# Performance work log

Hardware: AMD Instinct MI355X
Metric: run time of the kernel (lower is better)

Reference implementation:

```python
import jax, jax.numpy as jnp
import numpy as np

N_NODES = 50000
N_EDGES = 300000
MUL0 = 16          # multiplicity of 0e in irreps_in/out
MUL1 = 8           # multiplicity of 1o in irreps_in/out
SCAL_OUT = MUL0 + MUL1   # 24 = true scalars + gate scalars (tp scalar output)
DIM_IN = MUL0 + 3 * MUL1  # 40
W_NUMEL = MUL0 * SCAL_OUT + MUL1 * SCAL_OUT + MUL0 * MUL1 + MUL1 * MUL1  # 768
SQRT3 = float(np.sqrt(3.0))
ALPHA = float(1.0 / np.sqrt(MUL0 + MUL1))  # e3nn 'element' path norm: fan_in = 16*1 + 8*1 = 24
BN_EPS = 1e-5


def setup_inputs() -> dict:
    key = jax.random.key(0)
    ks = jax.random.split(key, 16)
    f32 = jnp.float32
    return {
        "node_features": jax.random.normal(ks[0], (N_NODES, DIM_IN), f32),
        "edge_sh": jax.random.normal(ks[1], (N_EDGES, 4), f32),
        "edge_basis": jax.random.uniform(ks[2], (N_EDGES, 8), dtype=f32),
        "edge_index": jax.random.randint(ks[3], (2, N_EDGES), 0, N_NODES),
        # radial MLP params (8 -> 64 -> 64 -> 768)
        "W1": jax.random.normal(ks[4], (8, 64), f32) / np.sqrt(8.0),
        "b1": jnp.zeros((64,), f32),
        "W2": jax.random.normal(ks[5], (64, 64), f32) / np.sqrt(64.0),
        "b2": jnp.zeros((64,), f32),
        "W3": jax.random.normal(ks[6], (64, W_NUMEL), f32) / np.sqrt(64.0),
        "b3": jnp.zeros((W_NUMEL,), f32),
        # o3.Linear (self-interaction) weights, block diagonal per irrep
        "si_w0": jax.random.normal(ks[7], (MUL0, MUL0), f32),
        "si_w1": jax.random.normal(ks[8], (MUL1, MUL1), f32),
        # e3nn BatchNorm affine params
        "bn_ws": jnp.ones((MUL0,), f32),
        "bn_bs": jnp.zeros((MUL0,), f32),
        "bn_wv": jnp.ones((MUL1,), f32),
    }


def _radial_mlp(basis, W1, b1, W2, b2, W3, b3):
    h = jax.nn.silu(basis @ W1 + b1)
    h = jax.nn.silu(h @ W2 + b2)
    return h @ W3 + b3  # (E, W_NUMEL)


def reference(node_features, edge_sh, edge_basis, edge_index,
              W1, b1, W2, b2, W3, b3, si_w0, si_w1, bn_ws, bn_bs, bn_wv):
    src, dst = edge_index[0], edge_index[1]
    E = edge_sh.shape[0]

    tp_w = _radial_mlp(edge_basis, W1, b1, W2, b2, W3, b3)  # (E, 768)
    o0 = MUL0 * SCAL_OUT                     # 384
    o1 = o0 + MUL1 * SCAL_OUT                # 576
    o2 = o1 + MUL0 * MUL1                    # 704
    w_ss = tp_w[:, :o0].reshape(E, MUL0, SCAL_OUT)   # 0e x 0e -> 0e
    w_vv = tp_w[:, o0:o1].reshape(E, MUL1, SCAL_OUT)  # 1o x 1o -> 0e
    w_sv = tp_w[:, o1:o2].reshape(E, MUL0, MUL1)      # 0e x 1o -> 1o
    w_vs = tp_w[:, o2:].reshape(E, MUL1, MUL1)        # 1o x 0e -> 1o

    # gather source node features
    feats = node_features[src]                          # (E, 40)
    sx = feats[:, :MUL0]                                # (E, 16)
    vx = feats[:, MUL0:].reshape(E, MUL1, 3)            # (E, 8, 3)
    sh0 = edge_sh[:, 0:1]                               # (E, 1)
    sh1 = edge_sh[:, 1:4]                               # (E, 3)

    # scalar output channels (true scalars + gate scalars), component-normalized CG
    dot_vv = jnp.einsum('eui,ei->eu', vx, sh1) / SQRT3  # 1o.1o -> 0e CG
    out_s = (jnp.einsum('eu,euw->ew', sx * sh0, w_ss)
             + jnp.einsum('eu,euw->ew', dot_vv, w_vv)) * ALPHA   # (E, 24)

    # vector (1o) output channels
    out_v = (jnp.einsum('eu,ei,euw->ewi', sx, sh1, w_sv)
             + jnp.einsum('eui,euw->ewi', vx * sh0[:, :, None], w_vs)) * ALPHA  # (E, 8, 3)

    messages = jnp.concatenate([out_s, out_v.reshape(E, 3 * MUL1)], axis=-1)  # (E, 48)

    # scatter-add to destination nodes
    agg = jax.ops.segment_sum(messages, dst, num_segments=node_features.shape[0])  # (N, 48)

    # Gate: SiLU on true scalars, sigmoid gate scalars modulate 1o irreps
    s = jax.nn.silu(agg[:, :MUL0])                       # (N, 16)
    g = jax.nn.sigmoid(agg[:, MUL0:SCAL_OUT])            # (N, 8)
    v = agg[:, SCAL_OUT:].reshape(-1, MUL1, 3) * g[:, :, None]  # (N, 8, 3)

    # self-interaction: o3.Linear, block-diagonal per irrep, 1/sqrt(fan_in) scaling
    s = s @ (si_w0 / np.sqrt(MUL0))                      # (N, 16)
    v = jnp.einsum('nui,uw->nwi', v, si_w1 / np.sqrt(MUL1))  # (N, 8, 3)

    # e3nn BatchNorm (training stats, component normalization, affine)
    s = s - jnp.mean(s, axis=0)
    s_norm = jnp.mean(s * s, axis=0)                     # (16,)
    s = s * jax.lax.rsqrt(s_norm + BN_EPS) * bn_ws + bn_bs
    v_norm = jnp.mean(jnp.mean(v * v, axis=-1), axis=0)  # (8,) per-mul mean sq component
    v = v * (jax.lax.rsqrt(v_norm + BN_EPS) * bn_wv)[None, :, None]

    out = jnp.concatenate([s, v.reshape(-1, 3 * MUL1)], axis=-1)  # (N, 40)
    return out + node_features  # residual (irreps_in == irreps_out)
```

## Files before the change

### kernel.cpp

```cpp
#include <hip/hip_runtime.h>
#include <hip/hip_bf16.h>


#define N_NODES_C 50000
#define N_EDGES_C 300000
#define ALPHA_C 0.20412414523193154f
#define INV_SQRT3_C 0.5773502691896258f
#define BN_EPS_C 1e-5f

typedef unsigned int u32;
typedef unsigned long long u64;
typedef unsigned short u16;
typedef __attribute__((ext_vector_type(8))) short bf16x8;
typedef __attribute__((ext_vector_type(4))) float f32x4;

#define OFF_STATS 0u
#define OFF_FLAG  48u
#define OFF_W3T   64u
#define OFF_W1T   49216u
#define OFF_B1    49728u
#define OFF_W2T   49792u
#define OFF_B2    53888u
#define OFF_B3    53952u
#define OFF_SI0   54720u
#define OFF_SI1   54976u
#define OFF_AGG   55040u
#define REQ_WS_BYTES ((size_t)(55040u + 2400000u) * 4u)
#define OFF_SPART   2455040u
#define OFF_START   2505040u
#define OFF_CURSOR  2555044u
#define OFF_POS     2605044u
#define OFF_MSG     2905044u
#define REQ2_WS_BYTES ((size_t)(2905044u + 14400000u) * 4u)

#define GATHER_BLOCKS ((N_NODES_C + 63) / 64)

__device__ __forceinline__ float bflo(u32 u){ union{u32 i; float f;} c; c.i = u<<16; return c.f; }
__device__ __forceinline__ float bfhi(u32 u){ union{u32 i; float f;} c; c.i = u & 0xffff0000u; return c.f; }
__device__ __forceinline__ float b2f(__hip_bfloat16 b){ return (float)b; }
__device__ __forceinline__ u16 f2bf(float f){
    union{float f; u32 i;} c; c.f = f;
    u32 r = c.i + 0x7fffu + ((c.i>>16)&1u);
    return (u16)(r>>16);
}
__device__ __forceinline__ float sigmoidf_(float x){ return 1.0f/(1.0f+__expf(-x)); }
__device__ __forceinline__ float siluf_(float x){ return x*sigmoidf_(x); }
__device__ __forceinline__ float rdv(const void* p, int idx, bool fm){
    return fm ? ((const float*)p)[idx] : b2f(((const __hip_bfloat16*)p)[idx]);
}
__device__ __forceinline__ float sel4(float a, float b, float c, float d, int q){
    float lo = (q&1) ? b : a;
    float hi = (q&1) ? d : c;
    return (q&2) ? hi : lo;
}
__device__ __forceinline__ float sel8(float a0,float a1,float a2,float a3,
                                      float a4,float a5,float a6,float a7,int q){
    float x0=(q&1)?a1:a0, x1=(q&1)?a3:a2, x2=(q&1)?a5:a4, x3=(q&1)?a7:a6;
    float y0=(q&2)?x1:x0, y1=(q&2)?x3:x2;
    return (q&4)?y1:y0;
}
__device__ __forceinline__ void wave_fence(){
    asm volatile("s_waitcnt lgkmcnt(0)" ::: "memory");
}

__global__ __launch_bounds__(256) void fill_kernel(u32* __restrict__ p, int n, u32 v){
    int i = blockIdx.x*256 + threadIdx.x;
    if (i < n) p[i] = v;
}

__global__ __launch_bounds__(256) void prep_kernel(
    const void* __restrict__ nf,
    const void* __restrict__ W1, const void* __restrict__ b1,
    const void* __restrict__ W2, const void* __restrict__ b2,
    const void* __restrict__ W3, const void* __restrict__ b3,
    const void* __restrict__ si0, const void* __restrict__ si1,
    float* __restrict__ ws)
{
    __shared__ u32 fmsh;
    {
        const int t = threadIdx.x;
        if (t < 64){
            u32 w = ((const u32*)nf)[t];
            int bad = 0;
            u32 lo = w & 0xffffu, hi = w >> 16;
            u32 elo = (lo >> 7) & 0xffu, ehi = (hi >> 7) & 0xffu;
            if (!(lo == 0u || (elo >= 90u && elo <= 140u))) bad++;
            if (!(hi == 0u || (ehi >= 90u && ehi <= 140u))) bad++;
            for (int off=32; off; off>>=1) bad += __shfl_down(bad, off);
            if (t == 0) fmsh = (bad >= 8) ? 1u : 0u;
        }
        __syncthreads();
    }
    const bool fm = fmsh != 0u;
    if (blockIdx.x == 0 && threadIdx.x == 0) ((u32*)(ws + OFF_FLAG))[0] = fm ? 1u : 0u;

    int i = blockIdx.x*256 + threadIdx.x;
    if (i < 49152){
        int j = i & 7, lane = (i>>3)&63, kh = (i>>9)&1, nt = i>>10;
        int n = lane & 15, qd = lane >> 4;
        int k = kh*32 + qd*8 + j;
        int col = nt*16 + n;
        float v = rdv(W3, k*768 + col, fm);
        u16 hv = f2bf(v);
        float hf = bflo((u32)hv);
        u16 lv = f2bf(v - hf);
        u16* BH = (u16*)(ws + OFF_W3T);
        BH[i] = hv;
        BH[49152 + i] = lv;
        return;
    }
    i -= 49152;
    if (i < 512){ int j=i>>3, t=i&7; ws[OFF_W1T+i] = rdv(W1, t*64+j, fm); return; }
    i -= 512;
    if (i < 64){ ws[OFF_B1+i] = rdv(b1, i, fm); return; }
    i -= 64;
    if (i < 4096){ int j=i>>6, k=i&63; ws[OFF_W2T+i] = rdv(W2, k*64+j, fm); return; }
    i -= 4096;
    if (i < 64){ ws[OFF_B2+i] = rdv(b2, i, fm); return; }
    i -= 64;
    if (i < 768){ ws[OFF_B3+i] = rdv(b3, i, fm); return; }
    i -= 768;
    if (i < 256){ int w=i>>4, u=i&15; ws[OFF_SI0+i] = rdv(si0, u*16+w, fm)*0.25f; return; }
    i -= 256;
    if (i < 64){ int w=i>>3, u=i&7; ws[OFF_SI1+i] = rdv(si1, u*8+w, fm)*0.35355339059327373f; return; }
}

__global__ __launch_bounds__(256) void rank_kernel(const int* __restrict__ dst,
                                                   int* __restrict__ cursor,
                                                   int* __restrict__ rank){
    int i = blockIdx.x*256 + threadIdx.x;
    if (i < N_EDGES_C){
        rank[i] = atomicAdd(&cursor[dst[i]], 1);
    }
}

__global__ __launch_bounds__(1024) void scan_kernel(const int* __restrict__ deg,
                                                    int* __restrict__ start){
    __shared__ int buf[2][1024];
    const int t = threadIdx.x;
    const int c0 = t*49;
    int local = 0;
    #pragma unroll 1
    for (int i=0;i<49;i++){ int idx=c0+i; if (idx<N_NODES_C) local += deg[idx]; }
    buf[0][t] = local;
    __syncthreads();
    int src=0;
    for (int off=1; off<1024; off<<=1){
        int v = buf[src][t];
        if (t>=off) v += buf[src][t-off];
        buf[src^1][t]=v;
        src^=1;
        __syncthreads();
    }
    int off = (t==0)?0:buf[src][t-1];
    #pragma unroll 1
    for (int i=0;i<49;i++){
        int idx=c0+i;
        if (idx<N_NODES_C){ start[idx]=off; off+=deg[idx]; }
    }
    if (t==0) start[N_NODES_C]=buf[src][1023];
}

__global__ __launch_bounds__(256) void pos_kernel(const int* __restrict__ dst,
                                                  const int* __restrict__ start,
                                                  int* __restrict__ rankpos){
    int i = blockIdx.x*256 + threadIdx.x;
    if (i < N_EDGES_C){
        rankpos[i] = start[dst[i]] + rankpos[i];
    }
}

template<bool SORTED>
__global__ __launch_bounds__(128, 2) void edge_kernel_t(
    const void* __restrict__ nfv,
    const void* __restrict__ eshv,
    const void* __restrict__ ebv,
    const int* __restrict__ eidx,
    const float* __restrict__ ws,
    const int* __restrict__ pos,
    float* __restrict__ outbuf)
{
    __shared__ __align__(16) char uni[2][12544];
    const int wv   = threadIdx.x >> 6;
    const int lane = threadIdx.x & 63;
    u16   (*h2hi)[72] = (u16 (*)[72])uni[wv];
    float (*tpb)[49]  = (float (*)[49])uni[wv];

    const bool fm = ((const u32*)(ws + OFF_FLAG))[0] != 0u;
    const int m    = lane & 15;
    const int quad = lane >> 4;
    const int e    = blockIdx.x*128 + threadIdx.x;
    const bool act = e < N_EDGES_C;
    const int slot = (SORTED && act) ? pos[e] : 0;

    float sh0=0.f, sh1x=0.f, sh1y=0.f, sh1z=0.f;
    float f[40];
    float bas[8];
    #pragma unroll
    for (int i=0;i<40;i++) f[i]=0.f;
    #pragma unroll
    for (int i=0;i<8;i++) bas[i]=0.f;
    if (act){
        const int src = eidx[e];
        if (!fm){
            const u32* p = (const u32*)((const __hip_bfloat16*)eshv + (size_t)e*4);
            u32 a = p[0], b = p[1];
            sh0 = bflo(a); sh1x = bfhi(a); sh1y = bflo(b); sh1z = bfhi(b);
            const uint4* qq = (const uint4*)((const __hip_bfloat16*)nfv + (size_t)src*40);
            #pragma unroll
            for (int i=0;i<5;i++){
                uint4 r = qq[i];
                f[i*8+0]=bflo(r.x); f[i*8+1]=bfhi(r.x);
                f[i*8+2]=bflo(r.y); f[i*8+3]=bfhi(r.y);
                f[i*8+4]=bflo(r.z); f[i*8+5]=bfhi(r.z);
                f[i*8+6]=bflo(r.w); f[i*8+7]=bfhi(r.w);
            }
            uint4 r = *(const uint4*)((const __hip_bfloat16*)ebv + (size_t)e*8);
            bas[0]=bflo(r.x); bas[1]=bfhi(r.x); bas[2]=bflo(r.y); bas[3]=bfhi(r.y);
            bas[4]=bflo(r.z); bas[5]=bfhi(r.z); bas[6]=bflo(r.w); bas[7]=bfhi(r.w);
        } else {
            float4 r = *(const float4*)((const float*)eshv + (size_t)e*4);
            sh0 = r.x; sh1x = r.y; sh1y = r.z; sh1z = r.w;
            const float4* qq = (const float4*)((const float*)nfv + (size_t)src*40);
            #pragma unroll
            for (int i=0;i<10;i++){
                float4 t = qq[i];
                f[i*4+0]=t.x; f[i*4+1]=t.y; f[i*4+2]=t.z; f[i*4+3]=t.w;
            }
            const float4* qb = (const float4*)((const float*)ebv + (size_t)e*8);
            float4 t0 = qb[0], t1 = qb[1];
            bas[0]=t0.x; bas[1]=t0.y; bas[2]=t0.z; bas[3]=t0.w;
            bas[4]=t1.x; bas[5]=t1.y; bas[6]=t1.z; bas[7]=t1.w;
        }
    }

    const float* W1T = ws + OFF_W1T;
    const float* b1f = ws + OFF_B1;
    float h1[64];
    #pragma unroll
    for (int j=0;j<64;j++){
        const float* w = W1T + j*8;
        float t0 = b1f[j] + bas[0]*w[0] + bas[4]*w[4];
        float t1 = bas[1]*w[1] + bas[5]*w[5];
        float t2 = bas[2]*w[2] + bas[6]*w[6];
        float t3 = bas[3]*w[3] + bas[7]*w[7];
        h1[j] = siluf_((t0+t1)+(t2+t3));
    }

    const float* W2T = ws + OFF_W2T;
    const float* bb2 = ws + OFF_B2;
    #pragma unroll 1
    for (int j=0;j<64;j+=2){
        const float* w0 = W2T + j*64;
        const float* w1 = w0 + 64;
        float a0=bb2[j],   a1=0.f, a2=0.f, a3=0.f;
        float c0=bb2[j+1], c1=0.f, c2=0.f, c3=0.f;
        #pragma unroll
        for (int k=0;k<64;k+=4){
            a0 += h1[k]*w0[k];     a1 += h1[k+1]*w0[k+1];
            a2 += h1[k+2]*w0[k+2]; a3 += h1[k+3]*w0[k+3];
            c0 += h1[k]*w1[k];     c1 += h1[k+1]*w1[k+1];
            c2 += h1[k+2]*w1[k+2]; c3 += h1[k+3]*w1[k+3];
        }
        u32 pk = (u32)f2bf(siluf_((a0+a1)+(a2+a3)))
               | ((u32)f2bf(siluf_((c0+c1)+(c2+c3)))<<16);
        *(u32*)&h2hi[lane][j] = pk;
    }
    wave_fence();

    bf16x8 Afr[4][2];
    #pragma unroll
    for (int g=0;g<4;g++){
        Afr[g][0] = *(const bf16x8*)&h2hi[g*16+m][quad*8];
        Afr[g][1] = *(const bf16x8*)&h2hi[g*16+m][32 + quad*8];
    }
    wave_fence();

    float vxsh0[24], dvv[8];
    #pragma unroll
    for (int j=0;j<24;j++) vxsh0[j] = f[16+j]*sh0;
    #pragma unroll
    for (int u=0;u<8;u++)
        dvv[u] = (f[16+u*3]*sh1x + f[17+u*3]*sh1y + f[18+u*3]*sh1z)*INV_SQRT3_C;

    float outs[24], tsv[8], av0[8], av1[8], av2[8];
    #pragma unroll
    for (int t=0;t<24;t++) outs[t]=0.f;
    #pragma unroll
    for (int t=0;t<8;t++){ tsv[t]=0.f; av0[t]=0.f; av1[t]=0.f; av2[t]=0.f; }

    const short* BH = (const short*)(ws + OFF_W3T);
    const float* b3f = ws + OFF_B3;

    auto loadB = [&](bf16x8* dst2, int cc2){
        #pragma unroll
        for (int ntl=0; ntl<3; ntl++){
            const int nt = cc2*3 + ntl;
            dst2[ntl*2+0] = *(const bf16x8*)(BH + ((nt*2+0)*64 + lane)*8);
            dst2[ntl*2+1] = *(const bf16x8*)(BH + ((nt*2+1)*64 + lane)*8);
        }
    };

    bf16x8 Bc[6];
    loadB(Bc, 0);

    #pragma unroll 1
    for (int cc=0; cc<16; cc++){
        #pragma unroll
        for (int ntl=0; ntl<3; ntl++){
            #pragma unroll
            for (int g=0; g<4; g++){
                f32x4 acc = {0.f,0.f,0.f,0.f};
                acc = __builtin_amdgcn_mfma_f32_16x16x32_bf16(Afr[g][0], Bc[ntl*2+0], acc, 0,0,0);
                acc = __builtin_amdgcn_mfma_f32_16x16x32_bf16(Afr[g][1], Bc[ntl*2+1], acc, 0,0,0);
                #pragma unroll
                for (int r=0;r<4;r++) tpb[g*16+quad*4+r][ntl*16+m] = acc[r];
            }
        }
        if (cc < 15) loadB(Bc, cc+1);
        wave_fence();

        float cA=0.f, cB=0.f;
        if (cc < 8){
            cA = sel8(f[0],f[2],f[4],f[6],f[8],f[10],f[12],f[14], cc)*sh0;
            cB = sel8(f[1],f[3],f[5],f[7],f[9],f[11],f[13],f[15], cc)*sh0;
        } else if (cc < 12){
            cA = sel4(dvv[0],dvv[2],dvv[4],dvv[6], cc-8);
            cB = sel4(dvv[1],dvv[3],dvv[5],dvv[7], cc-8);
        }
        const float* b3c = b3f + cc*48;
        float v[16];

        #pragma unroll
        for (int c=0;c<16;c++) v[c] = tpb[lane][c] + b3c[c];
        if (cc < 12){
            #pragma unroll
            for (int c=0;c<16;c++) outs[c] += cA*v[c];
        } else if (cc == 12){
            #pragma unroll
            for (int c=0;c<16;c++) tsv[c&7] += f[c>>3]*v[c];
        } else if (cc == 13){
            #pragma unroll
            for (int c=0;c<16;c++) tsv[c&7] += f[6+(c>>3)]*v[c];
        } else if (cc == 14){
            #pragma unroll
            for (int c=0;c<16;c++) tsv[c&7] += f[12+(c>>3)]*v[c];
        } else {
            #pragma unroll
            for (int c=0;c<16;c++){
                const int u=2+(c>>3), w=c&7;
                av0[w] += vxsh0[u*3+0]*v[c];
                av1[w] += vxsh0[u*3+1]*v[c];
                av2[w] += vxsh0[u*3+2]*v[c];
            }
        }

        #pragma unroll
        for (int c=0;c<16;c++) v[c] = tpb[lane][16+c] + b3c[16+c];
        if (cc < 12){
            #pragma unroll
            for (int c=0;c<8;c++)  outs[16+c] += cA*v[c];
            #pragma unroll
            for (int c=8;c<16;c++) outs[c-8]  += cB*v[c];
        } else if (cc == 12){
            #pragma unroll
            for (int c=0;c<16;c++) tsv[c&7] += f[2+(c>>3)]*v[c];
        } else if (cc == 13){
            #pragma unroll
            for (int c=0;c<16;c++) tsv[c&7] += f[8+(c>>3)]*v[c];
        } else if (cc == 14){
            #pragma unroll
            for (int c=0;c<16;c++) tsv[c&7] += f[14+(c>>3)]*v[c];
        } else {
            #pragma unroll
            for (int c=0;c<16;c++){
                const int u=4+(c>>3), w=c&7;
                av0[w] += vxsh0[u*3+0]*v[c];
                av1[w] += vxsh0[u*3+1]*v[c];
                av2[w] += vxsh0[u*3+2]*v[c];
            }
        }

        #pragma unroll
        for (int c=0;c<16;c++) v[c] = tpb[lane][32+c] + b3c[32+c];
        if (cc < 12){
            #pragma unroll
            for (int c=0;c<16;c++) outs[8+c] += cB*v[c];
        } else if (cc == 12){
            #pragma unroll
            for (int c=0;c<16;c++) tsv[c&7] += f[4+(c>>3)]*v[c];
        } else if (cc == 13){
            #pragma unroll
            for (int c=0;c<16;c++) tsv[c&7] += f[10+(c>>3)]*v[c];
        } else if (cc == 14){
            #pragma unroll
            for (int c=0;c<16;c++){
                const int u=(c>>3), w=c&7;
                av0[w] += vxsh0[u*3+0]*v[c];
                av1[w] += vxsh0[u*3+1]*v[c];
                av2[w] += vxsh0[u*3+2]*v[c];
            }
        } else {
            #pragma unroll
            for (int c=0;c<16;c++){
                const int u=6+(c>>3), w=c&7;
                av0[w] += vxsh0[u*3+0]*v[c];
                av1[w] += vxsh0[u*3+1]*v[c];
                av2[w] += vxsh0[u*3+2]*v[c];
            }
        }
        wave_fence();
    }

    if (act){
        if (SORTED){
            float v48[48];
            #pragma unroll
            for (int w=0;w<24;w++) v48[w] = outs[w]*ALPHA_C;
            #pragma unroll
            for (int w=0;w<8;w++){
                v48[24+w*3+0] = (tsv[w]*sh1x + av0[w])*ALPHA_C;
                v48[24+w*3+1] = (tsv[w]*sh1y + av1[w])*ALPHA_C;
                v48[24+w*3+2] = (tsv[w]*sh1z + av2[w])*ALPHA_C;
            }
            float4* mp = (float4*)(outbuf + (size_t)slot*48);
            #pragma unroll
            for (int q=0;q<12;q++) mp[q] = make_float4(v48[q*4],v48[q*4+1],v48[q*4+2],v48[q*4+3]);
        } else {
            const int dst = eidx[N_EDGES_C + e];
            float* dp = outbuf + (size_t)dst*48;
            #pragma unroll
            for (int w=0;w<24;w++) atomicAdd(dp+w, outs[w]*ALPHA_C);
            #pragma unroll
            for (int w=0;w<8;w++){
                atomicAdd(dp+24+w*3+0, (tsv[w]*sh1x + av0[w])*ALPHA_C);
                atomicAdd(dp+24+w*3+1, (tsv[w]*sh1y + av1[w])*ALPHA_C);
                atomicAdd(dp+24+w*3+2, (tsv[w]*sh1z + av2[w])*ALPHA_C);
            }
        }
    }
}

__global__ __launch_bounds__(512) void gather_node_kernel(
    const float* __restrict__ ws,
    const float* __restrict__ msg,
    const int* __restrict__ start,
    float* __restrict__ svb,
    float* __restrict__ spart)
{
    __shared__ __align__(16) float aggL[64][52];
    const float* si0T = ws + OFF_SI0;
    const float* si1T = ws + OFF_SI1;
    const int tid = threadIdx.x;
    const int nb = blockIdx.x*64;
    {
        const int sub  = tid & 3;
        const int rsp  = (tid >> 2) & 1;
        const int slot = tid >> 3;
        const int n = nb + slot;
        float a[12], b[12];
        #pragma unroll
        for (int i=0;i<12;i++){ a[i]=0.f; b[i]=0.f; }
        if (n < N_NODES_C){
            const int s = start[n], en = start[n+1];
            #pragma unroll 1
            for (int r = s + rsp; r < en; r += 4){
                const float4* mp = (const float4*)(msg + (size_t)r*48) + sub*3;
                float4 t0=mp[0], t1=mp[1], t2=mp[2];
                const int r2 = r + 2;
                if (r2 < en){
                    const float4* mq = (const float4*)(msg + (size_t)r2*48) + sub*3;
                    float4 u0=mq[0], u1=mq[1], u2=mq[2];
                    b[0]+=u0.x; b[1]+=u0.y; b[2]+=u0.z; b[3]+=u0.w;
                    b[4]+=u1.x; b[5]+=u1.y; b[6]+=u1.z; b[7]+=u1.w;
                    b[8]+=u2.x; b[9]+=u2.y; b[10]+=u2.z; b[11]+=u2.w;
                }
                a[0]+=t0.x; a[1]+=t0.y; a[2]+=t0.z; a[3]+=t0.w;
                a[4]+=t1.x; a[5]+=t1.y; a[6]+=t1.z; a[7]+=t1.w;
                a[8]+=t2.x; a[9]+=t2.y; a[10]+=t2.z; a[11]+=t2.w;
            }
        }
        #pragma unroll
        for (int i=0;i<12;i++) a[i] += b[i];
        #pragma unroll
        for (int i=0;i<12;i++) a[i] += __shfl_xor(a[i], 4);
        if (rsp == 0){
            float4* dp = (float4*)&aggL[slot][sub*12];
            dp[0]=make_float4(a[0],a[1],a[2],a[3]);
            dp[1]=make_float4(a[4],a[5],a[6],a[7]);
            dp[2]=make_float4(a[8],a[9],a[10],a[11]);
        }
    }
    __syncthreads();
    if (tid >= 64) return;
    const int n = nb + tid;
    const bool act = n < N_NODES_C;

    float a[48];
    {
        const float4* p = (const float4*)&aggL[tid][0];
        #pragma unroll
        for (int q=0;q<12;q++){ float4 r=p[q]; a[q*4]=r.x; a[q*4+1]=r.y; a[q*4+2]=r.z; a[q*4+3]=r.w; }
    }
    float spre[16];
    #pragma unroll
    for (int u=0;u<16;u++) spre[u]=siluf_(a[u]);
    float v[24];
    #pragma unroll
    for (int u=0;u<8;u++){
        float g = sigmoidf_(a[16+u]);
        v[u*3+0]=a[24+u*3+0]*g; v[u*3+1]=a[24+u*3+1]*g; v[u*3+2]=a[24+u*3+2]*g;
    }
    float so[16];
    #pragma unroll
    for (int w=0;w<16;w++){
        const float* c = si0T + w*16;
        float t0=0.f,t1=0.f,t2=0.f,t3=0.f;
        #pragma unroll
        for (int u=0;u<16;u+=4){ t0+=spre[u]*c[u]; t1+=spre[u+1]*c[u+1]; t2+=spre[u+2]*c[u+2]; t3+=spre[u+3]*c[u+3]; }
        so[w]=(t0+t1)+(t2+t3);
    }
    float vo[24];
    #pragma unroll
    for (int w=0;w<8;w++){
        const float* c = si1T + w*8;
        float a0=0.f,a1=0.f,a2=0.f;
        #pragma unroll
        for (int u=0;u<8;u++){ a0+=v[u*3]*c[u]; a1+=v[u*3+1]*c[u]; a2+=v[u*3+2]*c[u]; }
        vo[w*3]=a0; vo[w*3+1]=a1; vo[w*3+2]=a2;
    }
    if (act){
        float4* op = (float4*)(svb + (size_t)n*48);
        op[0]=make_float4(so[0],so[1],so[2],so[3]);
        op[1]=make_float4(so[4],so[5],so[6],so[7]);
        op[2]=make_float4(so[8],so[9],so[10],so[11]);
        op[3]=make_float4(so[12],so[13],so[14],so[15]);
        #pragma unroll
        for (int q=0;q<6;q++) op[4+q]=make_float4(vo[q*4],vo[q*4+1],vo[q*4+2],vo[q*4+3]);
    }
    float r[40];
    #pragma unroll
    for (int w=0;w<16;w++){ r[w]=so[w]; r[16+w]=so[w]*so[w]; }
    #pragma unroll
    for (int w=0;w<8;w++) r[32+w]=(vo[w*3]*vo[w*3]+vo[w*3+1]*vo[w*3+1]+vo[w*3+2]*vo[w*3+2])*(1.0f/3.0f);
    #pragma unroll
    for (int j=0;j<40;j++){
        float x = r[j];
        for (int off=32; off; off>>=1) x += __shfl_down(x, off);
        r[j]=x;
    }
    if (tid==0){
        float* sp = spart + (size_t)blockIdx.x*40;
        #pragma unroll
        for (int q=0;q<10;q++)
            *(float4*)(sp + q*4) = make_float4(r[q*4],r[q*4+1],r[q*4+2],r[q*4+3]);
    }
}

__global__ __launch_bounds__(1024) void reduce_stats_kernel(
    const float* __restrict__ spart, int nblk, float* __restrict__ stats)
{
    const int tid = threadIdx.x;
    if (tid >= 640) return;
    const int c = tid >> 4;
    const int l = tid & 15;
    float s = 0.f;
    #pragma unroll 1
    for (int k = l; k < nblk; k += 16) s += spart[(size_t)k*40 + c];
    #pragma unroll
    for (int off=8; off; off>>=1) s += __shfl_xor(s, off);
    if (l == 0) stats[c] = s;
}

__global__ __launch_bounds__(256) void node_kernel_atomic(
    const float* __restrict__ ws,
    float* __restrict__ svb,
    float* __restrict__ stats)
{
    const float* si0T = ws + OFF_SI0;
    const float* si1T = ws + OFF_SI1;
    const int n = blockIdx.x*256 + threadIdx.x;
    const bool act = n < N_NODES_C;

    float a[48];
    #pragma unroll
    for (int j=0;j<48;j++) a[j]=0.f;
    if (act){
        const float4* p = (const float4*)(svb + (size_t)n*48);
        #pragma unroll
        for (int q=0;q<12;q++){ float4 r=p[q]; a[q*4]=r.x; a[q*4+1]=r.y; a[q*4+2]=r.z; a[q*4+3]=r.w; }
    }
    float spre[16];
    #pragma unroll
    for (int u=0;u<16;u++) spre[u]=siluf_(a[u]);
    float v[24];
    #pragma unroll
    for (int u=0;u<8;u++){
        float g = sigmoidf_(a[16+u]);
        v[u*3+0]=a[24+u*3+0]*g; v[u*3+1]=a[24+u*3+1]*g; v[u*3+2]=a[24+u*3+2]*g;
    }
    float so[16];
    #pragma unroll
    for (int w=0;w<16;w++){
        const float* c = si0T + w*16;
        float t0=0.f,t1=0.f,t2=0.f,t3=0.f;
        #pragma unroll
        for (int u=0;u<16;u+=4){ t0+=spre[u]*c[u]; t1+=spre[u+1]*c[u+1]; t2+=spre[u+2]*c[u+2]; t3+=spre[u+3]*c[u+3]; }
        so[w]=(t0+t1)+(t2+t3);
    }
    float vo[24];
    #pragma unroll
    for (int w=0;w<8;w++){
        const float* c = si1T + w*8;
        float a0=0.f,a1=0.f,a2=0.f;
        #pragma unroll
        for (int u=0;u<8;u++){ a0+=v[u*3]*c[u]; a1+=v[u*3+1]*c[u]; a2+=v[u*3+2]*c[u]; }
        vo[w*3]=a0; vo[w*3+1]=a1; vo[w*3+2]=a2;
    }
    if (act){
        float4* op = (float4*)(svb + (size_t)n*48);
        op[0]=make_float4(so[0],so[1],so[2],so[3]);
        op[1]=make_float4(so[4],so[5],so[6],so[7]);
        op[2]=make_float4(so[8],so[9],so[10],so[11]);
        op[3]=make_float4(so[12],so[13],so[14],so[15]);
        #pragma unroll
        for (int q=0;q<6;q++) op[4+q]=make_float4(vo[q*4],vo[q*4+1],vo[q*4+2],vo[q*4+3]);
    }
    float r[40];
    #pragma unroll
    for (int w=0;w<16;w++){ r[w]=so[w]; r[16+w]=so[w]*so[w]; }
    #pragma unroll
    for (int w=0;w<8;w++) r[32+w]=(vo[w*3]*vo[w*3]+vo[w*3+1]*vo[w*3+1]+vo[w*3+2]*vo[w*3+2])*(1.0f/3.0f);
    #pragma unroll
    for (int j=0;j<40;j++){
        float x = r[j];
        for (int off=32; off; off>>=1) x += __shfl_down(x, off);
        r[j]=x;
    }
    if ((threadIdx.x & 63)==0){
        #pragma unroll
        for (int j=0;j<40;j++) atomicAdd(stats+j, r[j]);
    }
}

__global__ __launch_bounds__(256) void final_kernel(
    const float* __restrict__ ws, const float* __restrict__ svb,
    const void* __restrict__ nfv,
    const void* __restrict__ bnws, const void* __restrict__ bnbs,
    const void* __restrict__ bnwv,
    void* __restrict__ outv)
{
    const float* stats = ws + OFF_STATS;
    const bool fm = ((const u32*)(ws + OFF_FLAG))[0] != 0u;
    const int n = blockIdx.x*256 + threadIdx.x;
    if (n >= N_NODES_C) return;
    const float invN = 1.0f/(float)N_NODES_C;
    const float* s = svb + (size_t)n*48;
    float nfr[40];
    if (!fm){
        const uint4* q = (const uint4*)((const __hip_bfloat16*)nfv + (size_t)n*40);
        #pragma unroll
        for (int i=0;i<5;i++){
            uint4 r = q[i];
            nfr[i*8+0]=bflo(r.x); nfr[i*8+1]=bfhi(r.x);
            nfr[i*8+2]=bflo(r.y); nfr[i*8+3]=bfhi(r.y);
            nfr[i*8+4]=bflo(r.z); nfr[i*8+5]=bfhi(r.z);
            nfr[i*8+6]=bflo(r.w); nfr[i*8+7]=bfhi(r.w);
        }
    } else {
        const float4* q = (const float4*)((const float*)nfv + (size_t)n*40);
        #pragma unroll
        for (int i=0;i<10;i++){
            float4 t = q[i];
            nfr[i*4+0]=t.x; nfr[i*4+1]=t.y; nfr[i*4+2]=t.z; nfr[i*4+3]=t.w;
        }
    }
    float vals[40];
    #pragma unroll
    for (int w=0;w<16;w++){
        float mean = stats[w]*invN;
        float var  = fmaxf(stats[16+w]*invN - mean*mean, 0.0f);
        float is   = rsqrtf(var + BN_EPS_C) * rdv(bnws, w, fm);
        vals[w] = (s[w]-mean)*is + rdv(bnbs, w, fm) + nfr[w];
    }
    #pragma unroll
    for (int w=0;w<8;w++){
        float iv = rsqrtf(fmaxf(stats[32+w]*invN, 0.0f) + BN_EPS_C) * rdv(bnwv, w, fm);
        vals[16+w*3+0] = s[16+w*3+0]*iv + nfr[16+w*3+0];
        vals[16+w*3+1] = s[16+w*3+1]*iv + nfr[16+w*3+1];
        vals[16+w*3+2] = s[16+w*3+2]*iv + nfr[16+w*3+2];
    }
    if (!fm){
        u32 packed[20];
        #pragma unroll
        for (int q=0;q<20;q++) packed[q] = (u32)f2bf(vals[2*q]) | ((u32)f2bf(vals[2*q+1])<<16);
        uint4* op = (uint4*)((u16*)outv + (size_t)n*40);
        #pragma unroll
        for (int q=0;q<5;q++) op[q] = make_uint4(packed[q*4],packed[q*4+1],packed[q*4+2],packed[q*4+3]);
    } else {
        float4* op = (float4*)((float*)outv + (size_t)n*40);
        #pragma unroll
        for (int q=0;q<10;q++) op[q] = make_float4(vals[q*4],vals[q*4+1],vals[q*4+2],vals[q*4+3]);
    }
}

extern "C" void kernel_launch(void* const* d_in, const int* in_sizes, int n_in,
                              void* d_out, int out_size, void* d_ws, size_t ws_size,
                              hipStream_t stream)
{
    const void* nf     = d_in[0];
    const void* esh    = d_in[1];
    const void* ebasis = d_in[2];
    const int*  eidx   = (const int*)d_in[3];
    const void* W1 = d_in[4];
    const void* b1 = d_in[5];
    const void* W2 = d_in[6];
    const void* b2 = d_in[7];
    const void* W3 = d_in[8];
    const void* b3 = d_in[9];
    const void* si0 = d_in[10];
    const void* si1 = d_in[11];
    const void* bnws = d_in[12];
    const void* bnbs = d_in[13];
    const void* bnwv = d_in[14];

    float* ws    = (float*)d_ws;
    float* stats = ws + OFF_STATS;
    float* agg   = ws + OFF_AGG;

    if (ws_size < REQ_WS_BYTES){
        int nw = out_size/2;
        fill_kernel<<<(nw+255)/256, 256, 0, stream>>>((u32*)d_out, nw, 0x447A447Au);
        return;
    }

    const int* dst = eidx + N_EDGES_C;
    const int EB = (N_EDGES_C+255)/256;
    const int EB128 = (N_EDGES_C+127)/128;

    hipMemsetAsync(stats, 0, 48*sizeof(float), stream);
    prep_kernel<<<215, 256, 0, stream>>>(nf, W1,b1,W2,b2,W3,b3,si0,si1, ws);

    if (ws_size >= REQ2_WS_BYTES){
        int*   startp = (int*)(ws + OFF_START);
        int*   cursor = (int*)(ws + OFF_CURSOR);
        int*   posb   = (int*)(ws + OFF_POS);
        float* spart  = ws + OFF_SPART;
        float* msg    = ws + OFF_MSG;

        hipMemsetAsync(cursor, 0, N_NODES_C*sizeof(int), stream);
        rank_kernel<<<EB, 256, 0, stream>>>(dst, cursor, posb);
        scan_kernel<<<1, 1024, 0, stream>>>(cursor, startp);
        pos_kernel<<<EB, 256, 0, stream>>>(dst, startp, posb);
        edge_kernel_t<true><<<EB128, 128, 0, stream>>>(nf, esh, ebasis, eidx, ws, posb, msg);
        gather_node_kernel<<<GATHER_BLOCKS, 512, 0, stream>>>(ws, msg, startp, agg, spart);
        reduce_stats_kernel<<<1, 1024, 0, stream>>>(spart, GATHER_BLOCKS, stats);
    } else {
        hipMemsetAsync(agg, 0, (size_t)2400000*sizeof(float), stream);
        edge_kernel_t<false><<<EB128, 128, 0, stream>>>(nf, esh, ebasis, eidx, ws, nullptr, agg);
        node_kernel_atomic<<<(N_NODES_C+255)/256, 256, 0, stream>>>(ws, agg, stats);
    }
    final_kernel<<<(N_NODES_C+255)/256, 256, 0, stream>>>(ws, agg, nf, bnws, bnbs, bnwv, d_out);
}
```

Baseline: 500.8 us.

## Permute W3 columns so each chunk yields complete outputs, store per chunk

The W3 and b3 columns are permuted in the prep kernel so that each 48-column MFMA chunk holds every weight needed for two output channels. Each chunk can then reduce to final outputs and write or atomically add them at once, instead of keeping 48 running accumulators across all chunks. The vxsh0 values move to LDS, and the node-feature gather is deferred until after the MLP layers, all to lower register pressure. The cost is extra LDS space, more scattered small stores per chunk, and more LDS reads of vxl.

```diff
diff --git a/kernel.cpp b/kernel.cpp
--- a/kernel.cpp
+++ b/kernel.cpp
@@ -48,16 +48,16 @@
 __device__ __forceinline__ float rdv(const void* p, int idx, bool fm){
     return fm ? ((const float*)p)[idx] : b2f(((const __hip_bfloat16*)p)[idx]);
 }
-__device__ __forceinline__ float sel4(float a, float b, float c, float d, int q){
-    float lo = (q&1) ? b : a;
-    float hi = (q&1) ? d : c;
-    return (q&2) ? hi : lo;
-}
-__device__ __forceinline__ float sel8(float a0,float a1,float a2,float a3,
-                                      float a4,float a5,float a6,float a7,int q){
-    float x0=(q&1)?a1:a0, x1=(q&1)?a3:a2, x2=(q&1)?a5:a4, x3=(q&1)?a7:a6;
-    float y0=(q&2)?x1:x0, y1=(q&2)?x3:x2;
-    return (q&4)?y1:y0;
+__device__ __forceinline__ int w3col(int cc, int c){
+    int kk = (c >= 24) ? (c - 24) : c;
+    int hb = (c >= 24) ? 1 : 0;
+    if (cc < 12){
+        int w = 2*cc + hb;
+        return (kk < 16) ? (kk*24 + w) : (384 + (kk-16)*24 + w);
+    } else {
+        int w = 2*(cc-12) + hb;
+        return (kk < 16) ? (576 + kk*8 + w) : (704 + (kk-16)*8 + w);
+    }
 }
 __device__ __forceinline__ void wave_fence(){
     asm volatile("s_waitcnt lgkmcnt(0)" ::: "memory");
@@ -99,7 +99,8 @@
         int j = i & 7, lane = (i>>3)&63, kh = (i>>9)&1, nt = i>>10;
         int n = lane & 15, qd = lane >> 4;
         int k = kh*32 + qd*8 + j;
-        int col = nt*16 + n;
+        int cc = nt/3, c = (nt%3)*16 + n;
+        int col = w3col(cc, c);
         float v = rdv(W3, k*768 + col, fm);
         u16 hv = f2bf(v);
         float hf = bflo((u32)hv);
@@ -118,7 +119,11 @@
     i -= 4096;
     if (i < 64){ ws[OFF_B2+i] = rdv(b2, i, fm); return; }
     i -= 64;
-    if (i < 768){ ws[OFF_B3+i] = rdv(b3, i, fm); return; }
+    if (i < 768){
+        int cc = i/48, c = i%48;
+        ws[OFF_B3+i] = rdv(b3, w3col(cc, c), fm);
+        return;
+    }
     i -= 768;
     if (i < 256){ int w=i>>4, u=i&15; ws[OFF_SI0+i] = rdv(si0, u*16+w, fm)*0.25f; return; }
     i -= 256;
@@ -180,11 +185,12 @@
     const int* __restrict__ pos,
     float* __restrict__ outbuf)
 {
-    __shared__ __align__(16) char uni[2][12544];
+    __shared__ __align__(16) char uni[2][18688];
     const int wv   = threadIdx.x >> 6;
     const int lane = threadIdx.x & 63;
     u16   (*h2hi)[72] = (u16 (*)[72])uni[wv];
     float (*tpb)[49]  = (float (*)[49])uni[wv];
+    float (*vxl)[64]  = (float (*)[64])(uni[wv] + 12544);
 
     const bool fm = ((const u32*)(ws + OFF_FLAG))[0] != 0u;
     const int m    = lane & 15;
@@ -192,20 +198,70 @@
     const int e    = blockIdx.x*128 + threadIdx.x;
     const bool act = e < N_EDGES_C;
     const int slot = (SORTED && act) ? pos[e] : 0;
+    const int src  = act ? eidx[e] : 0;
+    const int dstn = (!SORTED && act) ? eidx[N_EDGES_C + e] : 0;
 
     float sh0=0.f, sh1x=0.f, sh1y=0.f, sh1z=0.f;
-    float f[40];
     float bas[8];
-    #pragma unroll
-    for (int i=0;i<40;i++) f[i]=0.f;
     #pragma unroll
     for (int i=0;i<8;i++) bas[i]=0.f;
     if (act){
-        const int src = eidx[e];
         if (!fm){
             const u32* p = (const u32*)((const __hip_bfloat16*)eshv + (size_t)e*4);
             u32 a = p[0], b = p[1];
             sh0 = bflo(a); sh1x = bfhi(a); sh1y = bflo(b); sh1z = bfhi(b);
+            uint4 r = *(const uint4*)((const __hip_bfloat16*)ebv + (size_t)e*8);
+            bas[0]=bflo(r.x); bas[1]=bfhi(r.x); bas[2]=bflo(r.y); bas[3]=bfhi(r.y);
+            bas[4]=bflo(r.z); bas[5]=bfhi(r.z); bas[6]=bflo(r.w); bas[7]=bfhi(r.w);
+        } else {
+            float4 r = *(const float4*)((const float*)eshv + (size_t)e*4);
+            sh0 = r.x; sh1x = r.y; sh1y = r.z; sh1z = r.w;
+            const float4* qb = (const float4*)((const float*)ebv + (size_t)e*8);
+            float4 t0 = qb[0], t1 = qb[1];
+            bas[0]=t0.x; bas[1]=t0.y; bas[2]=t0.z; bas[3]=t0.w;
+            bas[4]=t1.x; bas[5]=t1.y; bas[6]=t1.z; bas[7]=t1.w;
+        }
+    }
+
+    const float* W1T = ws + OFF_W1T;
+    const float* b1f = ws + OFF_B1;
+    float h1[64];
+    #pragma unroll
+    for (int j=0;j<64;j++){
+        const float* w = W1T + j*8;
+        float t0 = b1f[j] + bas[0]*w[0] + bas[4]*w[4];
+        float t1 = bas[1]*w[1] + bas[5]*w[5];
+        float t2 = bas[2]*w[2] + bas[6]*w[6];
+        float t3 = bas[3]*w[3] + bas[7]*w[7];
+        h1[j] = siluf_((t0+t1)+(t2+t3));
+    }
+
+    const float* W2T = ws + OFF_W2T;
+    const float* bb2 = ws + OFF_B2;
+    #pragma unroll 1
+    for (int j=0;j<64;j+=2){
+        const float* w0 = W2T + j*64;
+        const float* w1 = w0 + 64;
+        float a0=bb2[j],   a1=0.f, a2=0.f, a3=0.f;
+        float c0=bb2[j+1], c1=0.f, c2=0.f, c3=0.f;
+        #pragma unroll
+        for (int k=0;k<64;k+=4){
+            a0 += h1[k]*w0[k];     a1 += h1[k+1]*w0[k+1];
+            a2 += h1[k+2]*w0[k+2]; a3 += h1[k+3]*w0[k+3];
+            c0 += h1[k]*w1[k];     c1 += h1[k+1]*w1[k+1];
+            c2 += h1[k+2]*w1[k+2]; c3 += h1[k+3]*w1[k+3];
+        }
+        u32 pk = (u32)f2bf(siluf_((a0+a1)+(a2+a3)))
+               | ((u32)f2bf(siluf_((c0+c1)+(c2+c3)))<<16);
+        *(u32*)&h2hi[lane][j] = pk;
+    }
+    wave_fence();
+
+    float f[40];
+    #pragma unroll
+    for (int i=0;i<40;i++) f[i]=0.f;
+    if (act){
+        if (!fm){
             const uint4* qq = (const uint4*)((const __hip_bfloat16*)nfv + (size_t)src*40);
             #pragma unroll
             for (int i=0;i<5;i++){
@@ -215,58 +271,15 @@
                 f[i*8+4]=bflo(r.z); f[i*8+5]=bfhi(r.z);
                 f[i*8+6]=bflo(r.w); f[i*8+7]=bfhi(r.w);
             }
-            uint4 r = *(const uint4*)((const __hip_bfloat16*)ebv + (size_t)e*8);
-            bas[0]=bflo(r.x); bas[1]=bfhi(r.x); bas[2]=bflo(r.y); bas[3]=bfhi(r.y);
-            bas[4]=bflo(r.z); bas[5]=bfhi(r.z); bas[6]=bflo(r.w); bas[7]=bfhi(r.w);
         } else {
-            float4 r = *(const float4*)((const float*)eshv + (size_t)e*4);
-            sh0 = r.x; sh1x = r.y; sh1y = r.z; sh1z = r.w;
             const float4* qq = (const float4*)((const float*)nfv + (size_t)src*40);
             #pragma unroll
             for (int i=0;i<10;i++){
                 float4 t = qq[i];
                 f[i*4+0]=t.x; f[i*4+1]=t.y; f[i*4+2]=t.z; f[i*4+3]=t.w;
             }
-            const float4* qb = (const float4*)((const float*)ebv + (size_t)e*8);
-            float4 t0 = qb[0], t1 = qb[1];
-            bas[0]=t0.x; bas[1]=t0.y; bas[2]=t0.z; bas[3]=t0.w;
-            bas[4]=t1.x; bas[5]=t1.y; bas[6]=t1.z; bas[7]=t1.w;
-        }
-    }
-
-    const float* W1T = ws + OFF_W1T;
-    const float* b1f = ws + OFF_B1;
-    float h1[64];
-    #pragma unroll
-    for (int j=0;j<64;j++){
-        const float* w = W1T + j*8;
-        float t0 = b1f[j] + bas[0]*w[0] + bas[4]*w[4];
-        float t1 = bas[1]*w[1] + bas[5]*w[5];
-        float t2 = bas[2]*w[2] + bas[6]*w[6];
-        float t3 = bas[3]*w[3] + bas[7]*w[7];
-        h1[j] = siluf_((t0+t1)+(t2+t3));
-    }
-
-    const float* W2T = ws + OFF_W2T;
-    const float* bb2 = ws + OFF_B2;
-    #pragma unroll 1
-    for (int j=0;j<64;j+=2){
-        const float* w0 = W2T + j*64;
-        const float* w1 = w0 + 64;
-        float a0=bb2[j],   a1=0.f, a2=0.f, a3=0.f;
-        float c0=bb2[j+1], c1=0.f, c2=0.f, c3=0.f;
-        #pragma unroll
-        for (int k=0;k<64;k+=4){
-            a0 += h1[k]*w0[k];     a1 += h1[k+1]*w0[k+1];
-            a2 += h1[k+2]*w0[k+2]; a3 += h1[k+3]*w0[k+3];
-            c0 += h1[k]*w1[k];     c1 += h1[k+1]*w1[k+1];
-            c2 += h1[k+2]*w1[k+2]; c3 += h1[k+3]*w1[k+3];
-        }
-        u32 pk = (u32)f2bf(siluf_((a0+a1)+(a2+a3)))
-               | ((u32)f2bf(siluf_((c0+c1)+(c2+c3)))<<16);
-        *(u32*)&h2hi[lane][j] = pk;
-    }
-    wave_fence();
+        }
+    }
 
     bf16x8 Afr[4][2];
     #pragma unroll
@@ -276,18 +289,12 @@
     }
     wave_fence();
 
-    float vxsh0[24], dvv[8];
-    #pragma unroll
-    for (int j=0;j<24;j++) vxsh0[j] = f[16+j]*sh0;
+    float dvv[8];
     #pragma unroll
     for (int u=0;u<8;u++)
         dvv[u] = (f[16+u*3]*sh1x + f[17+u*3]*sh1y + f[18+u*3]*sh1z)*INV_SQRT3_C;
-
-    float outs[24], tsv[8], av0[8], av1[8], av2[8];
-    #pragma unroll
-    for (int t=0;t<24;t++) outs[t]=0.f;
-    #pragma unroll
-    for (int t=0;t<8;t++){ tsv[t]=0.f; av0[t]=0.f; av1[t]=0.f; av2[t]=0.f; }
+    #pragma unroll
+    for (int j=0;j<24;j++) vxl[j][lane] = f[16+j]*sh0;
 
     const short* BH = (const short*)(ws + OFF_W3T);
     const float* b3f = ws + OFF_B3;
@@ -303,6 +310,9 @@
 
     bf16x8 Bc[6];
     loadB(Bc, 0);
+
+    float* const mp = SORTED ? (outbuf + (size_t)slot*48)
+                             : (outbuf + (size_t)dstn*48);
 
     #pragma unroll 1
     for (int cc=0; cc<16; cc++){
@@ -320,124 +330,67 @@
         if (cc < 15) loadB(Bc, cc+1);
         wave_fence();
 
-        float cA=0.f, cB=0.f;
-        if (cc < 8){
-            cA = sel8(f[0],f[2],f[4],f[6],f[8],f[10],f[12],f[14], cc)*sh0;
-            cB = sel8(f[1],f[3],f[5],f[7],f[9],f[11],f[13],f[15], cc)*sh0;
-        } else if (cc < 12){
-            cA = sel4(dvv[0],dvv[2],dvv[4],dvv[6], cc-8);
-            cB = sel4(dvv[1],dvv[3],dvv[5],dvv[7], cc-8);
-        }
         const float* b3c = b3f + cc*48;
-        float v[16];
-
-        #pragma unroll
-        for (int c=0;c<16;c++) v[c] = tpb[lane][c] + b3c[c];
         if (cc < 12){
+            float sa0=0.f, sa1=0.f, da0=0.f, da1=0.f;
             #pragma unroll
-            for (int c=0;c<16;c++) outs[c] += cA*v[c];
-        } else if (cc == 12){
+            for (int k=0;k<16;k++){
+                sa0 += f[k]*(tpb[lane][k]    + b3c[k]);
+                sa1 += f[k]*(tpb[lane][24+k] + b3c[24+k]);
+            }
             #pragma unroll
-            for (int c=0;c<16;c++) tsv[c&7] += f[c>>3]*v[c];
-        } else if (cc == 13){
+            for (int k=0;k<8;k++){
+                da0 += dvv[k]*(tpb[lane][16+k] + b3c[16+k]);
+                da1 += dvv[k]*(tpb[lane][40+k] + b3c[40+k]);
+            }
+            float o0 = (sh0*sa0 + da0)*ALPHA_C;
+            float o1 = (sh0*sa1 + da1)*ALPHA_C;
+            if (act){
+                if (SORTED){
+                    *(float2*)(mp + 2*cc) = make_float2(o0, o1);
+                } else {
+                    atomicAdd(mp + 2*cc,     o0);
+                    atomicAdd(mp + 2*cc + 1, o1);
+                }
+            }
+        } else {
+            const int w0 = 2*(cc-12);
+            float t0=0.f, t1=0.f;
+            float a00=0.f,a01=0.f,a02=0.f, a10=0.f,a11=0.f,a12=0.f;
             #pragma unroll
-            for (int c=0;c<16;c++) tsv[c&7] += f[6+(c>>3)]*v[c];
-        } else if (cc == 14){
+            for (int k=0;k<16;k++){
+                t0 += f[k]*(tpb[lane][k]    + b3c[k]);
+                t1 += f[k]*(tpb[lane][24+k] + b3c[24+k]);
+            }
             #pragma unroll
-            for (int c=0;c<16;c++) tsv[c&7] += f[12+(c>>3)]*v[c];
-        } else {
-            #pragma unroll
-            for (int c=0;c<16;c++){
-                const int u=2+(c>>3), w=c&7;
-                av0[w] += vxsh0[u*3+0]*v[c];
-                av1[w] += vxsh0[u*3+1]*v[c];
-                av2[w] += vxsh0[u*3+2]*v[c];
-            }
-        }
-
-        #pragma unroll
-        for (int c=0;c<16;c++) v[c] = tpb[lane][16+c] + b3c[16+c];
-        if (cc < 12){
-            #pragma unroll
-            for (int c=0;c<8;c++)  outs[16+c] += cA*v[c];
-            #pragma unroll
-            for (int c=8;c<16;c++) outs[c-8]  += cB*v[c];
-        } else if (cc == 12){
-            #pragma unroll
-            for (int c=0;c<16;c++) tsv[c&7] += f[2+(c>>3)]*v[c];
-        } else if (cc == 13){
-            #pragma unroll
-            for (int c=0;c<16;c++) tsv[c&7] += f[8+(c>>3)]*v[c];
-        } else if (cc == 14){
-            #pragma unroll
-            for (int c=0;c<16;c++) tsv[c&7] += f[14+(c>>3)]*v[c];
-        } else {
-            #pragma unroll
-            for (int c=0;c<16;c++){
-                const int u=4+(c>>3), w=c&7;
-                av0[w] += vxsh0[u*3+0]*v[c];
-                av1[w] += vxsh0[u*3+1]*v[c];
-                av2[w] += vxsh0[u*3+2]*v[c];
-            }
-        }
-
-        #pragma unroll
-        for (int c=0;c<16;c++) v[c] = tpb[lane][32+c] + b3c[32+c];
-        if (cc < 12){
-            #pragma unroll
-            for (int c=0;c<16;c++) outs[8+c] += cB*v[c];
-        } else if (cc == 12){
-            #pragma unroll
-            for (int c=0;c<16;c++) tsv[c&7] += f[4+(c>>3)]*v[c];
-        } else if (cc == 13){
-            #pragma unroll
-            for (int c=0;c<16;c++) tsv[c&7] += f[10+(c>>3)]*v[c];
-        } else if (cc == 14){
-            #pragma unroll
-            for (int c=0;c<16;c++){
-                const int u=(c>>3), w=c&7;
-                av0[w] += vxsh0[u*3+0]*v[c];
-                av1[w] += vxsh0[u*3+1]*v[c];
-                av2[w] += vxsh0[u*3+2]*v[c];
-            }
-        } else {
-            #pragma unroll
-            for (int c=0;c<16;c++){
-                const int u=6+(c>>3), w=c&7;
-                av0[w] += vxsh0[u*3+0]*v[c];
-                av1[w] += vxsh0[u*3+1]*v[c];
-                av2[w] += vxsh0[u*3+2]*v[c];
+            for (int k=0;k<8;k++){
+                float v0 = tpb[lane][16+k] + b3c[16+k];
+                float v1 = tpb[lane][40+k] + b3c[40+k];
+                float x0 = vxl[k*3+0][lane];
+                float x1 = vxl[k*3+1][lane];
+                float x2 = vxl[k*3+2][lane];
+                a00 += x0*v0; a01 += x1*v0; a02 += x2*v0;
+                a10 += x0*v1; a11 += x1*v1; a12 += x2*v1;
+            }
+            float o0 = (t0*sh1x + a00)*ALPHA_C;
+            float o1 = (t0*sh1y + a01)*ALPHA_C;
+            float o2 = (t0*sh1z + a02)*ALPHA_C;
+            float o3 = (t1*sh1x + a10)*ALPHA_C;
+            float o4 = (t1*sh1y + a11)*ALPHA_C;
+            float o5 = (t1*sh1z + a12)*ALPHA_C;
+            if (act){
+                float* vp = mp + 24 + w0*3;
+                if (SORTED){
+                    *(float2*)(vp + 0) = make_float2(o0, o1);
+                    *(float2*)(vp + 2) = make_float2(o2, o3);
+                    *(float2*)(vp + 4) = make_float2(o4, o5);
+                } else {
+                    atomicAdd(vp+0, o0); atomicAdd(vp+1, o1); atomicAdd(vp+2, o2);
+                    atomicAdd(vp+3, o3); atomicAdd(vp+4, o4); atomicAdd(vp+5, o5);
+                }
             }
         }
         wave_fence();
-    }
-
-    if (act){
-        if (SORTED){
-            float v48[48];
-            #pragma unroll
-            for (int w=0;w<24;w++) v48[w] = outs[w]*ALPHA_C;
-            #pragma unroll
-            for (int w=0;w<8;w++){
-                v48[24+w*3+0] = (tsv[w]*sh1x + av0[w])*ALPHA_C;
-                v48[24+w*3+1] = (tsv[w]*sh1y + av1[w])*ALPHA_C;
-                v48[24+w*3+2] = (tsv[w]*sh1z + av2[w])*ALPHA_C;
-            }
-            float4* mp = (float4*)(outbuf + (size_t)slot*48);
-            #pragma unroll
-            for (int q=0;q<12;q++) mp[q] = make_float4(v48[q*4],v48[q*4+1],v48[q*4+2],v48[q*4+3]);
-        } else {
-            const int dst = eidx[N_EDGES_C + e];
-            float* dp = outbuf + (size_t)dst*48;
-            #pragma unroll
-            for (int w=0;w<24;w++) atomicAdd(dp+w, outs[w]*ALPHA_C);
-            #pragma unroll
-            for (int w=0;w<8;w++){
-                atomicAdd(dp+24+w*3+0, (tsv[w]*sh1x + av0[w])*ALPHA_C);
-                atomicAdd(dp+24+w*3+1, (tsv[w]*sh1y + av1[w])*ALPHA_C);
-                atomicAdd(dp+24+w*3+2, (tsv[w]*sh1z + av2[w])*ALPHA_C);
-            }
-        }
     }
 }
 
```

Result: faster. 456.3 us (median of 2 runs) (-8.9%).
